# Optimization experiments

Hardware: AMD Instinct MI355X
Metric: run time of the kernel (lower is better)

## Reference

```python
import jax, jax.numpy as jnp
import numpy as np

N = 100000          # nodes
E = 800000          # edges
H = 32              # hidden_features
L = 4               # num_layers
HS = 32             # hidden_edge_scores
EPS_BN = 1e-5
EPS_AGG = 1e-6


def _bn(x, g, b):
    # training-mode batch norm over the node/edge (batch) axis
    mu = jnp.mean(x, axis=0)
    var = jnp.var(x, axis=0)
    return (x - mu) * jax.lax.rsqrt(var + EPS_BN) * g + b


def setup_inputs() -> dict:
    key = jax.random.key(0)
    ks = jax.random.split(key, 24)
    rn = lambda k, s, sc=0.1: jax.random.normal(k, s, dtype=jnp.float32) * sc
    return {
        "x": rn(ks[0], (N, 1), 1.0),
        "e": rn(ks[1], (E, 1), 1.0),
        "edge_index": jax.random.randint(ks[2], (2, E), 0, N),
        # input projections
        "pe_w": rn(ks[3], (1, H)), "pe_b": rn(ks[4], (H,)),
        "ed_w": rn(ks[5], (1, H)), "ed_b": rn(ks[6], (H,)),
        # per-layer GatedGCN weights, stacked over layers
        "A_w": rn(ks[7], (L, H, H)), "A_b": rn(ks[8], (L, H)),
        "B_w": rn(ks[9], (L, H, H)), "B_b": rn(ks[10], (L, H)),
        "C_w": rn(ks[11], (L, H, H)), "C_b": rn(ks[12], (L, H)),
        "U_w": rn(ks[13], (L, H, H)), "U_b": rn(ks[14], (L, H)),
        "V_w": rn(ks[15], (L, H, H)), "V_b": rn(ks[16], (L, H)),
        # batch-norm affine params
        "bn_h_g": jnp.ones((L, H), jnp.float32), "bn_h_b": jnp.zeros((L, H), jnp.float32),
        "bn_e_g": jnp.ones((L, H), jnp.float32), "bn_e_b": jnp.zeros((L, H), jnp.float32),
        # score predictor: concat(src_h, dst_h, e) -> HS -> 1
        "W1_w": rn(ks[17], (3 * H, HS)), "W1_b": rn(ks[18], (HS,)),
        "W2_w": rn(ks[19], (HS, 1)), "W2_b": rn(ks[20], (1,)),
    }


def reference(x, e, edge_index, pe_w, pe_b, ed_w, ed_b,
              A_w, A_b, B_w, B_b, C_w, C_b, U_w, U_b, V_w, V_b,
              bn_h_g, bn_h_b, bn_e_g, bn_e_b, W1_w, W1_b, W2_w, W2_b):
    src, dst = edge_index[0], edge_index[1]
    h = x @ pe_w + pe_b          # [N, H]
    e = e @ ed_w + ed_b          # [E, H]
    n = h.shape[0]
    for l in range(L):
        Ah = h @ A_w[l] + A_b[l]
        Bh = h @ B_w[l] + B_b[l]
        Ce = e @ C_w[l] + C_b[l]
        Uh = h @ U_w[l] + U_b[l]
        Vh = h @ V_w[l] + V_b[l]
        # edge update: gather node features to edges
        e_new = Ah[dst] + Bh[src] + Ce               # [E, H]
        sigma = jax.nn.sigmoid(e_new)                # edge gates
        # gated mean aggregation: scatter-add to dst nodes
        num = jax.ops.segment_sum(sigma * Vh[src], dst, num_segments=n)
        den = jax.ops.segment_sum(sigma, dst, num_segments=n)
        h_new = Uh + num / (den + EPS_AGG)           # [N, H]
        # BN -> ReLU -> residual
        h = h + jax.nn.relu(_bn(h_new, bn_h_g[l], bn_h_b[l]))
        e = e + jax.nn.relu(_bn(e_new, bn_e_g[l], bn_e_b[l]))
    # score predictor over edges
    z = jnp.concatenate([h[src], h[dst], e], axis=1)  # [E, 3H]
    scores = jax.nn.relu(z @ W1_w + W1_b) @ W2_w + W2_b  # [E, 1]
    return scores
```

## Files before the change

### kernel.cpp

```cpp
#include <hip/hip_runtime.h>
#include <hip/hip_bf16.h>
#include <hip/hip_fp16.h>

#define NLAYERS 4
#define GRID_STRIDE 2048

typedef _Float16 half8_t __attribute__((ext_vector_type(8)));
typedef float float4_t __attribute__((ext_vector_type(4)));

__global__ void zero_ints(int* __restrict__ p, int n)
{
    int i = blockIdx.x * 256 + threadIdx.x;
    if (i < n) p[i] = 0;
}

__global__ void hist_kernel(const int* __restrict__ dsts, int* __restrict__ counts, int E)
{
    int i = blockIdx.x * 256 + threadIdx.x;
    if (i < E) atomicAdd(&counts[dsts[i]], 1);
}

__global__ __launch_bounds__(256) void scan1(const int* __restrict__ counts,
                                             int* __restrict__ offsets,
                                             int* __restrict__ blocksums, int N)
{
    __shared__ int sdata[256];
    int t = threadIdx.x;
    int bbase = blockIdx.x * 1024;
    int v[4]; int s = 0;
#pragma unroll
    for (int q = 0; q < 4; q++) {
        int idx = bbase + t * 4 + q;
        v[q] = (idx < N) ? counts[idx] : 0;
        s += v[q];
    }
    sdata[t] = s;
    __syncthreads();
    for (int off = 1; off < 256; off <<= 1) {
        int x = (t >= off) ? sdata[t - off] : 0;
        __syncthreads();
        sdata[t] += x;
        __syncthreads();
    }
    int excl = sdata[t] - s;
    int run = excl;
#pragma unroll
    for (int q = 0; q < 4; q++) {
        int idx = bbase + t * 4 + q;
        if (idx < N) offsets[idx] = run;
        run += v[q];
    }
    if (t == 255) blocksums[blockIdx.x] = sdata[255];
}

__global__ void scan2(int* __restrict__ blocksums, int nb)
{
    if (threadIdx.x == 0 && blockIdx.x == 0) {
        int run = 0;
        for (int b = 0; b < nb; b++) { int t = blocksums[b]; blocksums[b] = run; run += t; }
    }
}

__global__ void scan3(int* __restrict__ offsets, const int* __restrict__ blocksums,
                      int* __restrict__ cursor, int N)
{
    int i = blockIdx.x * 256 + threadIdx.x;
    if (i < N) {
        int v = offsets[i] + blocksums[i >> 10];
        offsets[i] = v;
        cursor[i] = v;
    }
}

__global__ void scatter_kernel(const int* __restrict__ srcs, const int* __restrict__ dsts,
                               int* __restrict__ cursor, int* __restrict__ perm,
                               int* __restrict__ srcp, int* __restrict__ dstp, int E)
{
    int i = blockIdx.x * 256 + threadIdx.x;
    if (i < E) {
        int d = dsts[i];
        int slot = atomicAdd(&cursor[d], 1);
        perm[slot] = i;
        srcp[slot] = srcs[i];
        dstp[slot] = d;
    }
}

__global__ void init_proj4(const float* __restrict__ in, const float* __restrict__ w,
                           const float* __restrict__ b, float4* __restrict__ out, size_t n4)
{
    size_t i = (size_t)blockIdx.x * 256 + threadIdx.x;
    if (i < n4) {
        int j4 = (int)(i & 7) * 4;
        float xv = in[i >> 3];
        float4 wv = *(const float4*)(w + j4);
        float4 bv = *(const float4*)(b + j4);
        out[i] = make_float4(fmaf(xv, wv.x, bv.x), fmaf(xv, wv.y, bv.y),
                             fmaf(xv, wv.z, bv.z), fmaf(xv, wv.w, bv.w));
    }
}

__global__ void init_ep16(const float* __restrict__ e_in, const int* __restrict__ perm,
                          const float* __restrict__ w, const float* __restrict__ b,
                          __half2* __restrict__ out, size_t n4)
{
    size_t i = (size_t)blockIdx.x * 256 + threadIdx.x;
    if (i < n4) {
        int row = (int)(i >> 3);
        float xv = e_in[perm[row]];
        int j4 = (int)(i & 7) * 4;
        float4 wv = *(const float4*)(w + j4);
        float4 bv = *(const float4*)(b + j4);
        out[i * 2]     = __floats2half2_rn(fmaf(xv, wv.x, bv.x), fmaf(xv, wv.y, bv.y));
        out[i * 2 + 1] = __floats2half2_rn(fmaf(xv, wv.z, bv.z), fmaf(xv, wv.w, bv.w));
    }
}

__device__ __forceinline__ void mat32(const float* __restrict__ hrow,
                                      const float* __restrict__ W, const float* __restrict__ Wb,
                                      float* __restrict__ dst)
{
    float acc[32];
#pragma unroll
    for (int j = 0; j < 32; j++) acc[j] = Wb[j];
#pragma unroll 4
    for (int k = 0; k < 32; k++) {
        float hk = hrow[k];
#pragma unroll
        for (int j = 0; j < 32; j++) acc[j] = fmaf(hk, W[k * 32 + j], acc[j]);
    }
    float4* o = (float4*)dst;
#pragma unroll
    for (int q = 0; q < 8; q++) o[q] = make_float4(acc[4*q], acc[4*q+1], acc[4*q+2], acc[4*q+3]);
}

__device__ __forceinline__ void mat32h(const float* __restrict__ hrow,
                                       const float* __restrict__ W, const float* __restrict__ Wb,
                                       __half* __restrict__ dst)
{
    float acc[32];
#pragma unroll
    for (int j = 0; j < 32; j++) acc[j] = Wb[j];
#pragma unroll 4
    for (int k = 0; k < 32; k++) {
        float hk = hrow[k];
#pragma unroll
        for (int j = 0; j < 32; j++) acc[j] = fmaf(hk, W[k * 32 + j], acc[j]);
    }
    __half2* o = (__half2*)dst;
#pragma unroll
    for (int q = 0; q < 16; q++) o[q] = __floats2half2_rn(acc[2*q], acc[2*q+1]);
}

__global__ __launch_bounds__(64) void node_gemm(
    const float* __restrict__ h,
    const float* __restrict__ Aw, const float* __restrict__ Ab,
    const float* __restrict__ Bw, const float* __restrict__ Bb,
    const float* __restrict__ Uw, const float* __restrict__ Ub,
    const float* __restrict__ Vw, const float* __restrict__ Vb,
    __half* __restrict__ Ahh, __half* __restrict__ Bhh,
    float* __restrict__ Uhh, __half* __restrict__ Vhh, int N)
{
    int nid = blockIdx.x * 64 + threadIdx.x;
    if (nid >= N) return;
    const float* hrow = h + (size_t)nid * 32;
    size_t o = (size_t)nid * 32;
    mat32h(hrow, Aw, Ab, Ahh + o);
    mat32h(hrow, Bw, Bb, Bhh + o);
    mat32(hrow, Uw, Ub, Uhh + o);
    mat32h(hrow, Vw, Vb, Vhh + o);
}

__global__ __launch_bounds__(256) void edge_en(
    const __half* __restrict__ ep,
    const int* __restrict__ srcp, const int* __restrict__ dstp,
    const __half* __restrict__ Ah, const __half* __restrict__ Bh,
    const float* __restrict__ Cw, const float* __restrict__ Cb,
    __half* __restrict__ enh, float* __restrict__ partial, int E)
{
    __shared__ float red[256];
    int tid = threadIdx.x;
    int lane = tid & 63;
    int m = lane & 15, q = lane >> 4;
    half8_t b0, b1;
#pragma unroll
    for (int i = 0; i < 8; i++) {
        int k = q * 8 + i;
        b0[i] = (_Float16)Cw[k * 32 + m];
        b1[i] = (_Float16)Cw[k * 32 + m + 16];
    }
    float cb0 = Cb[m], cb1 = Cb[m + 16];
    float es0 = 0.f, eq0 = 0.f, es1 = 0.f, eq1 = 0.f;

    int ntile = (E + 15) >> 4;
    int wid = blockIdx.x * 4 + (tid >> 6);
    int nwave = gridDim.x * 4;
    for (int t = wid; t < ntile; t += nwave) {
        int base = t << 4;
        int arow = base + m;
        if (arow >= E) arow = E - 1;
        half8_t a = *(const half8_t*)(ep + (size_t)arow * 32 + q * 8);
        float4_t acc0 = __builtin_amdgcn_mfma_f32_16x16x32_f16(a, b0, (float4_t){0.f,0.f,0.f,0.f}, 0, 0, 0);
        float4_t acc1 = __builtin_amdgcn_mfma_f32_16x16x32_f16(a, b1, (float4_t){0.f,0.f,0.f,0.f}, 0, 0, 0);
#pragma unroll
        for (int reg = 0; reg < 4; reg++) {
            int row = q * 4 + reg;
            int edge = base + row;
            if (edge < E) {
                int s = srcp[edge], d = dstp[edge];
                float ah0 = __half2float(Ah[(size_t)d * 32 + m]);
                float bh0 = __half2float(Bh[(size_t)s * 32 + m]);
                float ah1 = __half2float(Ah[(size_t)d * 32 + m + 16]);
                float bh1 = __half2float(Bh[(size_t)s * 32 + m + 16]);
                float en0 = acc0[reg] + cb0 + ah0 + bh0;
                float en1 = acc1[reg] + cb1 + ah1 + bh1;
                enh[(size_t)edge * 32 + m]      = __float2half_rn(en0);
                enh[(size_t)edge * 32 + m + 16] = __float2half_rn(en1);
                es0 += en0; eq0 += en0 * en0;
                es1 += en1; eq1 += en1 * en1;
            }
        }
    }
    float* p = partial + (size_t)blockIdx.x * 64;
    __syncthreads();
    red[tid] = es0;
    __syncthreads();
    if (tid < 16) {
        float s = 0.f;
#pragma unroll
        for (int w = 0; w < 4; w++)
#pragma unroll
            for (int k = 0; k < 4; k++) s += red[w * 64 + k * 16 + tid];
        p[tid] = s;
    }
    __syncthreads();
    red[tid] = es1;
    __syncthreads();
    if (tid < 16) {
        float s = 0.f;
#pragma unroll
        for (int w = 0; w < 4; w++)
#pragma unroll
            for (int k = 0; k < 4; k++) s += red[w * 64 + k * 16 + tid];
        p[16 + tid] = s;
    }
    __syncthreads();
    red[tid] = eq0;
    __syncthreads();
    if (tid < 16) {
        float s = 0.f;
#pragma unroll
        for (int w = 0; w < 4; w++)
#pragma unroll
            for (int k = 0; k < 4; k++) s += red[w * 64 + k * 16 + tid];
        p[32 + tid] = s;
    }
    __syncthreads();
    red[tid] = eq1;
    __syncthreads();
    if (tid < 16) {
        float s = 0.f;
#pragma unroll
        for (int w = 0; w < 4; w++)
#pragma unroll
            for (int k = 0; k < 4; k++) s += red[w * 64 + k * 16 + tid];
        p[48 + tid] = s;
    }
}

__global__ __launch_bounds__(256) void node_agg(
    const __half* __restrict__ enh, const int* __restrict__ srcp,
    const int* __restrict__ offsets, const int* __restrict__ counts,
    const __half* __restrict__ Vh, float* __restrict__ hnew,
    __half* __restrict__ ep, const float* __restrict__ sc_e, const float* __restrict__ sh_e,
    float* __restrict__ partial, int N)
{
    __shared__ float red[256];
    int tid = threadIdx.x, j = tid & 31, grp = tid >> 5;
    float sc = sc_e[j], sh = sh_e[j];
    float hsum = 0.f, hsq = 0.f;
    for (int nb0 = blockIdx.x * 8; nb0 < N; nb0 += gridDim.x * 8) {
        int node = nb0 + grp;
        if (node >= N) break;
        int start = offsets[node], len = counts[node];
        float num = 0.f, den = 0.f;
        int qq = 0;
        for (; qq + 2 <= len; qq += 2) {
            int p0 = start + qq, p1 = p0 + 1;
            int s0 = srcp[p0], s1 = srcp[p1];
            float en0 = __half2float(enh[(size_t)p0 * 32 + j]);
            float en1 = __half2float(enh[(size_t)p1 * 32 + j]);
            float vh0 = __half2float(Vh[(size_t)s0 * 32 + j]);
            float vh1 = __half2float(Vh[(size_t)s1 * 32 + j]);
            float sg0 = 1.f / (1.f + __expf(-en0));
            float sg1 = 1.f / (1.f + __expf(-en1));
            num = fmaf(sg0, vh0, num); num = fmaf(sg1, vh1, num);
            den += sg0 + sg1;
            float e0 = __half2float(ep[(size_t)p0 * 32 + j]);
            float e1 = __half2float(ep[(size_t)p1 * 32 + j]);
            ep[(size_t)p0 * 32 + j] = __float2half_rn(e0 + fmaxf(fmaf(en0, sc, sh), 0.f));
            ep[(size_t)p1 * 32 + j] = __float2half_rn(e1 + fmaxf(fmaf(en1, sc, sh), 0.f));
        }
        if (qq < len) {
            int p0 = start + qq;
            int s0 = srcp[p0];
            float en0 = __half2float(enh[(size_t)p0 * 32 + j]);
            float vh0 = __half2float(Vh[(size_t)s0 * 32 + j]);
            float sg0 = 1.f / (1.f + __expf(-en0));
            num = fmaf(sg0, vh0, num);
            den += sg0;
            float e0 = __half2float(ep[(size_t)p0 * 32 + j]);
            ep[(size_t)p0 * 32 + j] = __float2half_rn(e0 + fmaxf(fmaf(en0, sc, sh), 0.f));
        }
        size_t ho = (size_t)node * 32 + j;
        float hv = hnew[ho] + num / (den + 1e-6f);
        hnew[ho] = hv;
        hsum += hv; hsq += hv * hv;
    }
    __syncthreads();
    red[tid] = hsum;
    __syncthreads();
    float hS = 0.f;
    if (tid < 32) {
#pragma unroll
        for (int r = 0; r < 8; r++) hS += red[r * 32 + tid];
    }
    __syncthreads();
    red[tid] = hsq;
    __syncthreads();
    if (tid < 32) {
        float hQ = 0.f;
#pragma unroll
        for (int r = 0; r < 8; r++) hQ += red[r * 32 + tid];
        float* p = partial + (size_t)blockIdx.x * 64;
        p[tid] = hS; p[32 + tid] = hQ;
    }
}

__global__ __launch_bounds__(256) void stats_side(
    const float* __restrict__ partial, int nrows, double cnt,
    const float* __restrict__ g, const float* __restrict__ b,
    float* __restrict__ sc_out, float* __restrict__ sh_out)
{
    int j = blockIdx.x;
    __shared__ double rs[256], rq[256];
    double s = 0.0, q = 0.0;
    for (int r = threadIdx.x; r < nrows; r += 256) {
        s += (double)partial[(size_t)r * 64 + j];
        q += (double)partial[(size_t)r * 64 + 32 + j];
    }
    rs[threadIdx.x] = s; rq[threadIdx.x] = q;
    __syncthreads();
    for (int off = 128; off; off >>= 1) {
        if (threadIdx.x < off) { rs[threadIdx.x] += rs[threadIdx.x + off]; rq[threadIdx.x] += rq[threadIdx.x + off]; }
        __syncthreads();
    }
    if (threadIdx.x == 0) {
        double mean = rs[0] / cnt;
        double var = rq[0] / cnt - mean * mean;
        float scale = g[j] * (float)(1.0 / sqrt(var + 1e-5));
        sc_out[j] = scale;
        sh_out[j] = b[j] - (float)mean * scale;
    }
}

__global__ void apply4(const float4* __restrict__ pre, const float* __restrict__ scale,
                       const float* __restrict__ shift, float4* __restrict__ acc, size_t n4)
{
    size_t i = (size_t)blockIdx.x * 256 + threadIdx.x;
    if (i < n4) {
        int j4 = (int)(i & 7) * 4;
        float4 sc = *(const float4*)(scale + j4);
        float4 sh = *(const float4*)(shift + j4);
        float4 p = pre[i], a = acc[i];
        a.x += fmaxf(fmaf(p.x, sc.x, sh.x), 0.f);
        a.y += fmaxf(fmaf(p.y, sc.y, sh.y), 0.f);
        a.z += fmaxf(fmaf(p.z, sc.z, sh.z), 0.f);
        a.w += fmaxf(fmaf(p.w, sc.w, sh.w), 0.f);
        acc[i] = a;
    }
}

__global__ void apply4_h16(const float4* __restrict__ pre, const float* __restrict__ scale,
                           const float* __restrict__ shift, const float4* __restrict__ hold,
                           __half2* __restrict__ h16, size_t n4)
{
    size_t i = (size_t)blockIdx.x * 256 + threadIdx.x;
    if (i < n4) {
        int j4 = (int)(i & 7) * 4;
        float4 sc = *(const float4*)(scale + j4);
        float4 sh = *(const float4*)(shift + j4);
        float4 p = pre[i], a = hold[i];
        a.x += fmaxf(fmaf(p.x, sc.x, sh.x), 0.f);
        a.y += fmaxf(fmaf(p.y, sc.y, sh.y), 0.f);
        a.z += fmaxf(fmaf(p.z, sc.z, sh.z), 0.f);
        a.w += fmaxf(fmaf(p.w, sc.w, sh.w), 0.f);
        h16[i * 2]     = __floats2half2_rn(a.x, a.y);
        h16[i * 2 + 1] = __floats2half2_rn(a.z, a.w);
    }
}

__global__ __launch_bounds__(256) void predictor(
    const __half* __restrict__ h16, const __half* __restrict__ e16,
    const int* __restrict__ srcp, const int* __restrict__ dstp, const int* __restrict__ perm,
    const float* __restrict__ W1, const float* __restrict__ b1,
    const float* __restrict__ W2, const float* __restrict__ b2v,
    float* __restrict__ out, int E)
{
    int tid = threadIdx.x;
    int lane = tid & 63;
    int m = lane & 15, q = lane >> 4;
    half8_t bf00, bf01, bf10, bf11, bf20, bf21;
#pragma unroll
    for (int i = 0; i < 8; i++) {
        int k = q * 8 + i;
        bf00[i] = (_Float16)W1[k * 32 + m];
        bf01[i] = (_Float16)W1[k * 32 + m + 16];
        bf10[i] = (_Float16)W1[(32 + k) * 32 + m];
        bf11[i] = (_Float16)W1[(32 + k) * 32 + m + 16];
        bf20[i] = (_Float16)W1[(64 + k) * 32 + m];
        bf21[i] = (_Float16)W1[(64 + k) * 32 + m + 16];
    }
    float b10 = b1[m], b11 = b1[m + 16];
    float w20 = W2[m], w21 = W2[m + 16];
    float b2 = b2v[0];

    int ntile = (E + 15) >> 4;
    int wid = blockIdx.x * 4 + (tid >> 6);
    int nwave = gridDim.x * 4;
    for (int t = wid; t < ntile; t += nwave) {
        int base = t << 4;
        int arow = base + m;
        if (arow >= E) arow = E - 1;
        int s = srcp[arow], d = dstp[arow];
        half8_t a0 = *(const half8_t*)(h16 + (size_t)s * 32 + q * 8);
        half8_t a1 = *(const half8_t*)(h16 + (size_t)d * 32 + q * 8);
        half8_t a2 = *(const half8_t*)(e16 + (size_t)arow * 32 + q * 8);
        float4_t acc0 = {0.f, 0.f, 0.f, 0.f}, acc1 = {0.f, 0.f, 0.f, 0.f};
        acc0 = __builtin_amdgcn_mfma_f32_16x16x32_f16(a0, bf00, acc0, 0, 0, 0);
        acc1 = __builtin_amdgcn_mfma_f32_16x16x32_f16(a0, bf01, acc1, 0, 0, 0);
        acc0 = __builtin_amdgcn_mfma_f32_16x16x32_f16(a1, bf10, acc0, 0, 0, 0);
        acc1 = __builtin_amdgcn_mfma_f32_16x16x32_f16(a1, bf11, acc1, 0, 0, 0);
        acc0 = __builtin_amdgcn_mfma_f32_16x16x32_f16(a2, bf20, acc0, 0, 0, 0);
        acc1 = __builtin_amdgcn_mfma_f32_16x16x32_f16(a2, bf21, acc1, 0, 0, 0);
#pragma unroll
        for (int reg = 0; reg < 4; reg++) {
            float tp = fmaxf(acc0[reg] + b10, 0.f) * w20
                     + fmaxf(acc1[reg] + b11, 0.f) * w21;
            tp += __shfl_xor(tp, 1);
            tp += __shfl_xor(tp, 2);
            tp += __shfl_xor(tp, 4);
            tp += __shfl_xor(tp, 8);
            int edge = base + q * 4 + reg;
            if (m == 0 && edge < E) out[perm[edge]] = tp + b2;
        }
    }
}

extern "C" void kernel_launch(void* const* d_in, const int* in_sizes, int n_in,
                              void* d_out, int out_size, void* d_ws, size_t ws_size,
                              hipStream_t stream)
{
    const int N = in_sizes[0];
    const int E = in_sizes[1];

    const float* x    = (const float*)d_in[0];
    const float* e_in = (const float*)d_in[1];
    const int*   eidx = (const int*)d_in[2];
    const float* pe_w = (const float*)d_in[3];
    const float* pe_b = (const float*)d_in[4];
    const float* ed_w = (const float*)d_in[5];
    const float* ed_b = (const float*)d_in[6];
    const float* Aw = (const float*)d_in[7];
    const float* Ab = (const float*)d_in[8];
    const float* Bw = (const float*)d_in[9];
    const float* Bb = (const float*)d_in[10];
    const float* Cw = (const float*)d_in[11];
    const float* Cb = (const float*)d_in[12];
    const float* Uw = (const float*)d_in[13];
    const float* Ub = (const float*)d_in[14];
    const float* Vw = (const float*)d_in[15];
    const float* Vb = (const float*)d_in[16];
    const float* bn_h_g = (const float*)d_in[17];
    const float* bn_h_b = (const float*)d_in[18];
    const float* bn_e_g = (const float*)d_in[19];
    const float* bn_e_b = (const float*)d_in[20];
    const float* W1w = (const float*)d_in[21];
    const float* W1b = (const float*)d_in[22];
    const float* W2w = (const float*)d_in[23];
    const float* W2b = (const float*)d_in[24];

    const int* srcs = eidx;
    const int* dsts = eidx + E;

    size_t nh = (size_t)N * 32;
    size_t eh = (size_t)E * 32;

    float* ws = (float*)d_ws;
    float* stats     = ws;
    float* partial_h = stats + 128;
    float* partial_e = partial_h + GRID_STRIDE * 64;
    float* h    = partial_e + GRID_STRIDE * 64;
    float* hnew = h + nh;
    __half* Ah  = (__half*)(hnew + nh);
    __half* Bh  = Ah + nh;
    __half* Vh  = Bh + nh;
    __half* ep  = Vh + nh;
    __half* enh = ep + eh;
    int* counts    = (int*)(enh + eh);
    int* offsets   = counts + N;
    int* cursor    = offsets + N;
    int* blocksums = cursor + N;
    int* perm      = blocksums + 128;
    int* srcp      = perm + E;
    int* dstp      = srcp + E;

    size_t nh4 = nh / 4, eh4 = eh / 4;
    int gh4 = (int)((nh4 + 255) / 256);
    int ge4 = (int)((eh4 + 255) / 256);
    int gN = (N + 255) / 256;
    int gE = (E + 255) / 256;
    int nb = (N + 1023) / 1024;

    zero_ints<<<gN, 256, 0, stream>>>(counts, N);
    hist_kernel<<<gE, 256, 0, stream>>>(dsts, counts, E);
    scan1<<<nb, 256, 0, stream>>>(counts, offsets, blocksums, N);
    scan2<<<1, 64, 0, stream>>>(blocksums, nb);
    scan3<<<gN, 256, 0, stream>>>(offsets, blocksums, cursor, N);
    scatter_kernel<<<gE, 256, 0, stream>>>(srcs, dsts, cursor, perm, srcp, dstp, E);

    init_proj4<<<gh4, 256, 0, stream>>>(x, pe_w, pe_b, (float4*)h, nh4);
    init_ep16<<<ge4, 256, 0, stream>>>(e_in, perm, ed_w, ed_b, (__half2*)ep, eh4);

    for (int l = 0; l < NLAYERS; l++) {
        node_gemm<<<(N + 63) / 64, 64, 0, stream>>>(h,
            Aw + l * 1024, Ab + l * 32,
            Bw + l * 1024, Bb + l * 32,
            Uw + l * 1024, Ub + l * 32,
            Vw + l * 1024, Vb + l * 32,
            Ah, Bh, hnew, Vh, N);
        edge_en<<<GRID_STRIDE, 256, 0, stream>>>(ep, srcp, dstp, Ah, Bh,
            Cw + l * 1024, Cb + l * 32, enh, partial_e, E);
        stats_side<<<32, 256, 0, stream>>>(partial_e, GRID_STRIDE, (double)E,
            bn_e_g + l * 32, bn_e_b + l * 32, stats + 64, stats + 96);
        node_agg<<<GRID_STRIDE, 256, 0, stream>>>(enh, srcp, offsets, counts,
            Vh, hnew, ep, stats + 64, stats + 96, partial_h, N);
        stats_side<<<32, 256, 0, stream>>>(partial_h, GRID_STRIDE, (double)N,
            bn_h_g + l * 32, bn_h_b + l * 32, stats + 0, stats + 32);
        if (l < NLAYERS - 1)
            apply4<<<gh4, 256, 0, stream>>>((const float4*)hnew, stats + 0, stats + 32,
                                            (float4*)h, nh4);
        else
            apply4_h16<<<gh4, 256, 0, stream>>>((const float4*)hnew, stats + 0, stats + 32,
                                                (const float4*)h, (__half2*)Ah, nh4);
    }

    predictor<<<GRID_STRIDE, 256, 0, stream>>>((const __half*)Ah, (const __half*)ep,
                                               srcp, dstp, perm, W1w, W1b, W2w, W2b,
                                               (float*)d_out, E);
}
```

Baseline: 788.0 us.

## Defer edge residual update into next layer's edge_en and predictor

The edge-feature residual update (BN+ReLU+add), previously done with scattered per-element half stores inside node_agg, now happens in the next layer's edge_en, which already streams ep. It uses vectorized 16-byte loads and writes there, and the predictor applies the final layer's update on the fly. This removes a read-modify-write pass from the latency-bound aggregation kernel, but edge_en gains an extra read of enh and a write of ep. Separately, the CSR scatter is split into an atomic permutation kernel plus a coalesced-write gather of src/dst.

```diff
diff --git a/kernel.cpp b/kernel.cpp
--- a/kernel.cpp
+++ b/kernel.cpp
@@ -72,17 +72,25 @@
     }
 }
 
-__global__ void scatter_kernel(const int* __restrict__ srcs, const int* __restrict__ dsts,
-                               int* __restrict__ cursor, int* __restrict__ perm,
-                               int* __restrict__ srcp, int* __restrict__ dstp, int E)
+__global__ void scatter_perm(const int* __restrict__ dsts, int* __restrict__ cursor,
+                             int* __restrict__ perm, int E)
 {
     int i = blockIdx.x * 256 + threadIdx.x;
     if (i < E) {
-        int d = dsts[i];
-        int slot = atomicAdd(&cursor[d], 1);
+        int slot = atomicAdd(&cursor[dsts[i]], 1);
         perm[slot] = i;
-        srcp[slot] = srcs[i];
-        dstp[slot] = d;
+    }
+}
+
+__global__ void gather_sd(const int* __restrict__ perm, const int* __restrict__ srcs,
+                          const int* __restrict__ dsts, int* __restrict__ srcp,
+                          int* __restrict__ dstp, int E)
+{
+    int i = blockIdx.x * 256 + threadIdx.x;
+    if (i < E) {
+        int e = perm[i];
+        srcp[i] = srcs[e];
+        dstp[i] = dsts[e];
     }
 }
 
@@ -171,8 +179,10 @@
     mat32h(hrow, Vw, Vb, Vhh + o);
 }
 
+template <int FUSE>
 __global__ __launch_bounds__(256) void edge_en(
-    const __half* __restrict__ ep,
+    __half* __restrict__ ep,
+    const float* __restrict__ sc_e, const float* __restrict__ sh_e,
     const int* __restrict__ srcp, const int* __restrict__ dstp,
     const __half* __restrict__ Ah, const __half* __restrict__ Bh,
     const float* __restrict__ Cw, const float* __restrict__ Cb,
@@ -183,11 +193,13 @@
     int lane = tid & 63;
     int m = lane & 15, q = lane >> 4;
     half8_t b0, b1;
+    float sc8[8], sh8[8];
 #pragma unroll
     for (int i = 0; i < 8; i++) {
         int k = q * 8 + i;
         b0[i] = (_Float16)Cw[k * 32 + m];
         b1[i] = (_Float16)Cw[k * 32 + m + 16];
+        if (FUSE) { sc8[i] = sc_e[k]; sh8[i] = sh_e[k]; }
     }
     float cb0 = Cb[m], cb1 = Cb[m + 16];
     float es0 = 0.f, eq0 = 0.f, es1 = 0.f, eq1 = 0.f;
@@ -198,8 +210,21 @@
     for (int t = wid; t < ntile; t += nwave) {
         int base = t << 4;
         int arow = base + m;
-        if (arow >= E) arow = E - 1;
-        half8_t a = *(const half8_t*)(ep + (size_t)arow * 32 + q * 8);
+        bool valid = arow < E;
+        if (!valid) arow = E - 1;
+        half8_t a;
+        if (FUSE) {
+            half8_t epv = *(const half8_t*)(ep + (size_t)arow * 32 + q * 8);
+            half8_t env = *(const half8_t*)(enh + (size_t)arow * 32 + q * 8);
+#pragma unroll
+            for (int i = 0; i < 8; i++) {
+                float e = (float)epv[i] + fmaxf(fmaf((float)env[i], sc8[i], sh8[i]), 0.f);
+                a[i] = (_Float16)e;
+            }
+            if (valid) *(half8_t*)(ep + (size_t)arow * 32 + q * 8) = a;
+        } else {
+            a = *(const half8_t*)(ep + (size_t)arow * 32 + q * 8);
+        }
         float4_t acc0 = __builtin_amdgcn_mfma_f32_16x16x32_f16(a, b0, (float4_t){0.f,0.f,0.f,0.f}, 0, 0, 0);
         float4_t acc1 = __builtin_amdgcn_mfma_f32_16x16x32_f16(a, b1, (float4_t){0.f,0.f,0.f,0.f}, 0, 0, 0);
 #pragma unroll
@@ -272,12 +297,10 @@
     const __half* __restrict__ enh, const int* __restrict__ srcp,
     const int* __restrict__ offsets, const int* __restrict__ counts,
     const __half* __restrict__ Vh, float* __restrict__ hnew,
-    __half* __restrict__ ep, const float* __restrict__ sc_e, const float* __restrict__ sh_e,
     float* __restrict__ partial, int N)
 {
     __shared__ float red[256];
     int tid = threadIdx.x, j = tid & 31, grp = tid >> 5;
-    float sc = sc_e[j], sh = sh_e[j];
     float hsum = 0.f, hsq = 0.f;
     for (int nb0 = blockIdx.x * 8; nb0 < N; nb0 += gridDim.x * 8) {
         int node = nb0 + grp;
@@ -296,10 +319,6 @@
             float sg1 = 1.f / (1.f + __expf(-en1));
             num = fmaf(sg0, vh0, num); num = fmaf(sg1, vh1, num);
             den += sg0 + sg1;
-            float e0 = __half2float(ep[(size_t)p0 * 32 + j]);
-            float e1 = __half2float(ep[(size_t)p1 * 32 + j]);
-            ep[(size_t)p0 * 32 + j] = __float2half_rn(e0 + fmaxf(fmaf(en0, sc, sh), 0.f));
-            ep[(size_t)p1 * 32 + j] = __float2half_rn(e1 + fmaxf(fmaf(en1, sc, sh), 0.f));
         }
         if (qq < len) {
             int p0 = start + qq;
@@ -309,8 +328,6 @@
             float sg0 = 1.f / (1.f + __expf(-en0));
             num = fmaf(sg0, vh0, num);
             den += sg0;
-            float e0 = __half2float(ep[(size_t)p0 * 32 + j]);
-            ep[(size_t)p0 * 32 + j] = __float2half_rn(e0 + fmaxf(fmaf(en0, sc, sh), 0.f));
         }
         size_t ho = (size_t)node * 32 + j;
         float hv = hnew[ho] + num / (den + 1e-6f);
@@ -401,7 +418,9 @@
 }
 
 __global__ __launch_bounds__(256) void predictor(
-    const __half* __restrict__ h16, const __half* __restrict__ e16,
+    const __half* __restrict__ h16, const __half* __restrict__ ep,
+    const __half* __restrict__ enh,
+    const float* __restrict__ sc_e, const float* __restrict__ sh_e,
     const int* __restrict__ srcp, const int* __restrict__ dstp, const int* __restrict__ perm,
     const float* __restrict__ W1, const float* __restrict__ b1,
     const float* __restrict__ W2, const float* __restrict__ b2v,
@@ -411,6 +430,7 @@
     int lane = tid & 63;
     int m = lane & 15, q = lane >> 4;
     half8_t bf00, bf01, bf10, bf11, bf20, bf21;
+    float sc8[8], sh8[8];
 #pragma unroll
     for (int i = 0; i < 8; i++) {
         int k = q * 8 + i;
@@ -420,6 +440,7 @@
         bf11[i] = (_Float16)W1[(32 + k) * 32 + m + 16];
         bf20[i] = (_Float16)W1[(64 + k) * 32 + m];
         bf21[i] = (_Float16)W1[(64 + k) * 32 + m + 16];
+        sc8[i] = sc_e[k]; sh8[i] = sh_e[k];
     }
     float b10 = b1[m], b11 = b1[m + 16];
     float w20 = W2[m], w21 = W2[m + 16];
@@ -435,7 +456,14 @@
         int s = srcp[arow], d = dstp[arow];
         half8_t a0 = *(const half8_t*)(h16 + (size_t)s * 32 + q * 8);
         half8_t a1 = *(const half8_t*)(h16 + (size_t)d * 32 + q * 8);
-        half8_t a2 = *(const half8_t*)(e16 + (size_t)arow * 32 + q * 8);
+        half8_t epv = *(const half8_t*)(ep + (size_t)arow * 32 + q * 8);
+        half8_t env = *(const half8_t*)(enh + (size_t)arow * 32 + q * 8);
+        half8_t a2;
+#pragma unroll
+        for (int i = 0; i < 8; i++) {
+            float e = (float)epv[i] + fmaxf(fmaf((float)env[i], sc8[i], sh8[i]), 0.f);
+            a2[i] = (_Float16)e;
+        }
         float4_t acc0 = {0.f, 0.f, 0.f, 0.f}, acc1 = {0.f, 0.f, 0.f, 0.f};
         acc0 = __builtin_amdgcn_mfma_f32_16x16x32_f16(a0, bf00, acc0, 0, 0, 0);
         acc1 = __builtin_amdgcn_mfma_f32_16x16x32_f16(a0, bf01, acc1, 0, 0, 0);
@@ -527,7 +555,8 @@
     scan1<<<nb, 256, 0, stream>>>(counts, offsets, blocksums, N);
     scan2<<<1, 64, 0, stream>>>(blocksums, nb);
     scan3<<<gN, 256, 0, stream>>>(offsets, blocksums, cursor, N);
-    scatter_kernel<<<gE, 256, 0, stream>>>(srcs, dsts, cursor, perm, srcp, dstp, E);
+    scatter_perm<<<gE, 256, 0, stream>>>(dsts, cursor, perm, E);
+    gather_sd<<<gE, 256, 0, stream>>>(perm, srcs, dsts, srcp, dstp, E);
 
     init_proj4<<<gh4, 256, 0, stream>>>(x, pe_w, pe_b, (float4*)h, nh4);
     init_ep16<<<ge4, 256, 0, stream>>>(e_in, perm, ed_w, ed_b, (__half2*)ep, eh4);
@@ -539,12 +568,16 @@
             Uw + l * 1024, Ub + l * 32,
             Vw + l * 1024, Vb + l * 32,
             Ah, Bh, hnew, Vh, N);
-        edge_en<<<GRID_STRIDE, 256, 0, stream>>>(ep, srcp, dstp, Ah, Bh,
-            Cw + l * 1024, Cb + l * 32, enh, partial_e, E);
+        if (l == 0)
+            edge_en<0><<<GRID_STRIDE, 256, 0, stream>>>(ep, stats + 64, stats + 96,
+                srcp, dstp, Ah, Bh, Cw + l * 1024, Cb + l * 32, enh, partial_e, E);
+        else
+            edge_en<1><<<GRID_STRIDE, 256, 0, stream>>>(ep, stats + 64, stats + 96,
+                srcp, dstp, Ah, Bh, Cw + l * 1024, Cb + l * 32, enh, partial_e, E);
         stats_side<<<32, 256, 0, stream>>>(partial_e, GRID_STRIDE, (double)E,
             bn_e_g + l * 32, bn_e_b + l * 32, stats + 64, stats + 96);
         node_agg<<<GRID_STRIDE, 256, 0, stream>>>(enh, srcp, offsets, counts,
-            Vh, hnew, ep, stats + 64, stats + 96, partial_h, N);
+            Vh, hnew, partial_h, N);
         stats_side<<<32, 256, 0, stream>>>(partial_h, GRID_STRIDE, (double)N,
             bn_h_g + l * 32, bn_h_b + l * 32, stats + 0, stats + 32);
         if (l < NLAYERS - 1)
@@ -556,6 +589,7 @@
     }
 
     predictor<<<GRID_STRIDE, 256, 0, stream>>>((const __half*)Ah, (const __half*)ep,
+                                               (const __half*)enh, stats + 64, stats + 96,
                                                srcp, dstp, perm, W1w, W1b, W2w, W2b,
                                                (float*)d_out, E);
 }
```

New measurement: 845.8 us. 1.07x slower.
